# Kernel optimization log

Hardware: AMD Instinct MI355X
Metric: run time of the kernel (lower is better)

Reference implementation:

```python
import jax, jax.numpy as jnp
import numpy as np

P = 9          # patch_size (hardcoded in module)
P2 = P * P     # 81


def _conv1x1(t, W, b):
    # t: (B, C, D, H, W); 1x1x1 Conv3d == per-voxel channel mix
    return jnp.einsum('bcdhw,oc->bodhw', t, W) + b[None, :, None, None, None]


def _unfold_patches(t, nD, nW):
    # t: (C, D, HW) -> non-overlapping P x P patches, torch.nn.Unfold ordering
    C = t.shape[0]
    t = t.reshape(C, nD, P, nW, P)            # (C, pd, kd, pw, kw)
    t = t.transpose(0, 1, 3, 2, 4)            # (C, pd, pw, kd, kw)
    return t.reshape(C, nD * nW, P2)          # (C, L, 81)


def _res_trans(v, W1, W2):
    # Sequential(Linear(81->162, no bias), Linear(162->81, no bias), LeakyReLU(0.2))
    h = jnp.einsum('clk,mk->clm', v, W1)      # (C, L, 162)
    h = jnp.einsum('clm,km->clk', h, W2)      # (C, L, 81)
    return jax.nn.leaky_relu(h, negative_slope=0.2)


def setup_inputs() -> dict:
    key = jax.random.key(0)
    ks = jax.random.split(key, 8)
    B, C, D, H, W = 1, 32, 36, 48, 48
    return {
        'x': jax.random.normal(ks[0], (B, C, D, H, W), jnp.float32),
        'y': jax.random.normal(ks[1], (B, C, D, H, W), jnp.float32),
        'W_img': jax.random.normal(ks[2], (C, C), jnp.float32) * 0.05,
        'b_img': jax.random.normal(ks[3], (C,), jnp.float32) * 0.05,
        'W_fea': jax.random.normal(ks[4], (C, C), jnp.float32) * 0.05,
        'b_fea': jax.random.normal(ks[5], (C,), jnp.float32) * 0.05,
        'W1': jax.random.normal(ks[6], (2 * P2, P2), jnp.float32) * 0.05,
        'W2': jax.random.normal(ks[7], (P2, 2 * P2), jnp.float32) * 0.05,
    }


def reference(x, y, W_img, b_img, W_fea, b_fea, W1, W2):
    B, C, D, H, W = x.shape
    HW = H * W
    nD, nW = D // P, HW // P
    xc = _conv1x1(x, W_img, b_img).reshape(C, D, HW)
    yc = _conv1x1(y, W_fea, b_fea).reshape(C, D, HW)
    px = _res_trans(_unfold_patches(xc, nD, nW), W1, W2)   # (C, L, 81)
    py = _res_trans(_unfold_patches(yc, nD, nW), W1, W2)   # (C, L, 81)
    # att[c, l1, l2] = <px[c,l1], py[c,l2]> / 81  (vectorized over channels)
    att = jnp.einsum('clk,cmk->clm', px, py) / P2           # (C, L, L)
    return att[None]                                        # (1, C, L, L)
```

## Files before the change

kernel.cpp:

```cpp
#include <hip/hip_runtime.h>
#include <hip/hip_bf16.h>

typedef unsigned short u16;
using short8  = __attribute__((ext_vector_type(8))) short;
using floatx4 = __attribute__((ext_vector_type(4))) float;

#define KPAD 104
#define VSTR 96

__device__ __forceinline__ u16 f2bf(float f) {
  union { float f; unsigned u; } v; v.f = f;
  unsigned r = v.u + 0x7fffu + ((v.u >> 16) & 1u);
  return (u16)(r >> 16);
}

__global__ __launch_bounds__(256) void k_conv(const float* __restrict__ xg,
                                              const float* __restrict__ yg,
                                              const float* __restrict__ Wi,
                                              const float* __restrict__ bi,
                                              const float* __restrict__ Wf,
                                              const float* __restrict__ bfe,
                                              const float* __restrict__ W1,
                                              const float* __restrict__ W2,
                                              u16* __restrict__ V,
                                              u16* __restrict__ wepad) {
  int t = threadIdx.x;
  if (blockIdx.y == 2) {
    if (blockIdx.x >= 39) return;
    int idx = blockIdx.x * 256 + t;
    int kp = idx / 104, k = idx - kp * 104;
    float s = 0.f;
    if (kp < 81 && k < 81) {
      #pragma unroll 6
      for (int m = 0; m < 162; ++m)
        s = fmaf(W2[kp * 162 + m], W1[m * 81 + k], s);
    }
    wepad[idx] = (kp < 81 && k < 81) ? f2bf(s) : (u16)0;
    return;
  }
  __shared__ float Ws[1024];
  __shared__ float bs[32];
  int tensor = blockIdx.y;
  const float* src = tensor ? yg : xg;
  const float* Wg  = tensor ? Wf : Wi;
  const float* bg  = tensor ? bfe : bi;
  for (int i = t; i < 1024; i += 256) Ws[i] = Wg[i];
  if (t < 32) bs[t] = bg[t];
  __syncthreads();

  int vbase = blockIdx.x * 512 + t;
  float xin[2][32];
  #pragma unroll
  for (int c = 0; c < 32; ++c) {
    xin[0][c] = src[c * 82944 + vbase];
    xin[1][c] = src[c * 82944 + vbase + 256];
  }
  int dst[2];
  #pragma unroll
  for (int v = 0; v < 2; ++v) {
    int vox = vbase + v * 256;
    int d  = vox / 2304, hw = vox - d * 2304;
    int pd = d / 9,  kd = d  - pd * 9;
    int pw = hw / 9, kw = hw - pw * 9;
    dst[v] = tensor * (32 * 1024 * VSTR) + (pd * 256 + pw) * VSTR + kd * 9 + kw;
  }
  #pragma unroll
  for (int o = 0; o < 32; ++o) {
    float s0 = bs[o], s1 = bs[o];
    #pragma unroll
    for (int c = 0; c < 32; ++c) {
      float w = Ws[o * 32 + c];
      s0 = fmaf(w, xin[0][c], s0);
      s1 = fmaf(w, xin[1][c], s1);
    }
    V[dst[0] + o * (1024 * VSTR)] = f2bf(s0);
    V[dst[1] + o * (1024 * VSTR)] = f2bf(s1);
  }
}

__global__ __launch_bounds__(256, 2) void k_att(const u16* __restrict__ V,
                                                const u16* __restrict__ wepad,
                                                float* __restrict__ out) {
  __shared__ u16 WeT[96 * KPAD];
  __shared__ u16 pxs[128 * KPAD];
  __shared__ u16 pys[128 * KPAD];
  int t = threadIdx.x;
  int c = blockIdx.z;
  int l1b = blockIdx.y * 128, l2b = blockIdx.x * 128;
  const u16* vx = V + ((c)      * 1024 + l1b) * VSTR;
  const u16* vy = V + ((32 + c) * 1024 + l2b) * VSTR;

  for (int i = t; i < 1248; i += 256)
    *(short8*)&WeT[i * 8] = ((const short8*)wepad)[i];
  for (int i = t; i < 1536; i += 256) {
    int r = i / 12, xx = i - r * 12;
    short8 a = *(const short8*)&vx[i * 8];
    short8 b = *(const short8*)&vy[i * 8];
    *(short8*)&pxs[r * KPAD + xx * 8] = a;
    *(short8*)&pys[r * KPAD + xx * 8] = b;
  }
  __syncthreads();

  int wave = t >> 6, lane = t & 63;
  int m15 = lane & 15, quad = lane >> 4;

  short8 bw[6][3];
  #pragma unroll
  for (int j = 0; j < 6; ++j)
    #pragma unroll
    for (int ks = 0; ks < 3; ++ks)
      bw[j][ks] = *(const short8*)&WeT[(j * 16 + m15) * KPAD + ks * 32 + quad * 8];

  int wbase = wave * 32;
  #pragma unroll
  for (int tz = 0; tz < 2; ++tz) {
    u16* buf = tz ? pys : pxs;
    short8 a[2][3];
    #pragma unroll
    for (int i2 = 0; i2 < 2; ++i2)
      #pragma unroll
      for (int ks = 0; ks < 3; ++ks)
        a[i2][ks] = *(const short8*)&buf[(wbase + i2 * 16 + m15) * KPAD + ks * 32 + quad * 8];
    floatx4 pacc[2][6];
    #pragma unroll
    for (int i2 = 0; i2 < 2; ++i2)
      #pragma unroll
      for (int j = 0; j < 6; ++j) pacc[i2][j] = (floatx4){0.f, 0.f, 0.f, 0.f};
    #pragma unroll
    for (int ks = 0; ks < 3; ++ks)
      #pragma unroll
      for (int i2 = 0; i2 < 2; ++i2)
        #pragma unroll
        for (int j = 0; j < 6; ++j)
          pacc[i2][j] = __builtin_amdgcn_mfma_f32_16x16x32_bf16(a[i2][ks], bw[j][ks], pacc[i2][j], 0, 0, 0);
    #pragma unroll
    for (int i2 = 0; i2 < 2; ++i2)
      #pragma unroll
      for (int j = 0; j < 6; ++j)
        #pragma unroll
        for (int reg = 0; reg < 4; ++reg) {
          int row = wbase + i2 * 16 + quad * 4 + reg;
          int col = j * 16 + m15;
          float v = pacc[i2][j][reg];
          v = v > 0.f ? v : 0.2f * v;
          buf[row * KPAD + col] = f2bf(v);
        }
  }
  __syncthreads();

  int wy = (wave >> 1) * 64, wx = (wave & 1) * 64;
  floatx4 acc[4][4];
  #pragma unroll
  for (int i = 0; i < 4; ++i)
    #pragma unroll
    for (int j = 0; j < 4; ++j) acc[i][j] = (floatx4){0.f, 0.f, 0.f, 0.f};

  #pragma unroll
  for (int ks = 0; ks < 3; ++ks) {
    short8 a[4], b[4];
    #pragma unroll
    for (int i = 0; i < 4; ++i)
      a[i] = *(const short8*)&pxs[(wy + i * 16 + m15) * KPAD + ks * 32 + quad * 8];
    #pragma unroll
    for (int j = 0; j < 4; ++j)
      b[j] = *(const short8*)&pys[(wx + j * 16 + m15) * KPAD + ks * 32 + quad * 8];
    #pragma unroll
    for (int i = 0; i < 4; ++i)
      #pragma unroll
      for (int j = 0; j < 4; ++j)
        acc[i][j] = __builtin_amdgcn_mfma_f32_16x16x32_bf16(a[i], b[j], acc[i][j], 0, 0, 0);
  }

  const float inv = 1.f / 81.f;
  #pragma unroll
  for (int i = 0; i < 4; ++i)
    #pragma unroll
    for (int j = 0; j < 4; ++j)
      #pragma unroll
      for (int reg = 0; reg < 4; ++reg) {
        int row = l1b + wy + i * 16 + quad * 4 + reg;
        int col = l2b + wx + j * 16 + m15;
        out[(c << 20) + (row << 10) + col] = acc[i][j][reg] * inv;
      }
}

extern "C" void kernel_launch(void* const* d_in, const int* in_sizes, int n_in,
                              void* d_out, int out_size, void* d_ws, size_t ws_size,
                              hipStream_t stream) {
  const float* x    = (const float*)d_in[0];
  const float* y    = (const float*)d_in[1];
  const float* Wimg = (const float*)d_in[2];
  const float* bimg = (const float*)d_in[3];
  const float* Wfea = (const float*)d_in[4];
  const float* bfea = (const float*)d_in[5];
  const float* W1   = (const float*)d_in[6];
  const float* W2   = (const float*)d_in[7];
  float* out = (float*)d_out;

  char* ws = (char*)d_ws;
  u16* wepad = (u16*)ws;
  u16* V     = (u16*)(ws + 32768);

  hipMemsetAsync(V, 0, 65536 * (size_t)VSTR * 2, stream);
  k_conv<<<dim3(162, 3), 256, 0, stream>>>(x, y, Wimg, bimg, Wfea, bfea, W1, W2, V, wepad);
  k_att<<<dim3(8, 8, 32), 256, 0, stream>>>(V, wepad, out);
}
```

Baseline: 205.4 us.

## Fuse patch projection into conv kernel and drop memset from pipeline

Moves the per-patch Linear+LeakyReLU projection out of the attention kernel and into a new fused conv kernel that computes the 1x1 conv for 4 patches per block directly into shared memory, projects them with MFMA and writes the projected patches to global. The attention kernel then only loads the precomputed patches and does the final GEMM. Previously each projection was recomputed 8 times across attention tiles. The change also removes the workspace memset by zeroing the padding in shared memory, and raises attention occupancy to 3 blocks per CU. It adds a third launch and uses strided, less coalesced input reads in the fused conv.

New measurement: 201.7 us. Within noise of the previous version (-1.8%).

```diff
diff --git a/kernel.cpp b/kernel.cpp
--- a/kernel.cpp
+++ b/kernel.cpp
@@ -1,5 +1,4 @@
 #include <hip/hip_runtime.h>
-#include <hip/hip_bf16.h>
 
 typedef unsigned short u16;
 using short8  = __attribute__((ext_vector_type(8))) short;
@@ -14,84 +13,132 @@
   return (u16)(r >> 16);
 }
 
-__global__ __launch_bounds__(256) void k_conv(const float* __restrict__ xg,
-                                              const float* __restrict__ yg,
-                                              const float* __restrict__ Wi,
-                                              const float* __restrict__ bi,
-                                              const float* __restrict__ Wf,
-                                              const float* __restrict__ bfe,
-                                              const float* __restrict__ W1,
+__global__ __launch_bounds__(256) void k_weff(const float* __restrict__ W1,
                                               const float* __restrict__ W2,
-                                              u16* __restrict__ V,
                                               u16* __restrict__ wepad) {
-  int t = threadIdx.x;
-  if (blockIdx.y == 2) {
-    if (blockIdx.x >= 39) return;
-    int idx = blockIdx.x * 256 + t;
-    int kp = idx / 104, k = idx - kp * 104;
-    float s = 0.f;
-    if (kp < 81 && k < 81) {
-      #pragma unroll 6
-      for (int m = 0; m < 162; ++m)
-        s = fmaf(W2[kp * 162 + m], W1[m * 81 + k], s);
-    }
-    wepad[idx] = (kp < 81 && k < 81) ? f2bf(s) : (u16)0;
-    return;
-  }
+  int idx = blockIdx.x * 256 + threadIdx.x;
+  if (idx >= 96 * 104) return;
+  int kp = idx / 104, k = idx - kp * 104;
+  float s = 0.f;
+  if (kp < 81 && k < 81) {
+    #pragma unroll 6
+    for (int m = 0; m < 162; ++m)
+      s = fmaf(W2[kp * 162 + m], W1[m * 81 + k], s);
+  }
+  wepad[idx] = (kp < 81 && k < 81) ? f2bf(s) : (u16)0;
+}
+
+__global__ __launch_bounds__(256, 2) void k_fused(const float* __restrict__ xg,
+                                                  const float* __restrict__ yg,
+                                                  const float* __restrict__ Wi,
+                                                  const float* __restrict__ bi,
+                                                  const float* __restrict__ Wf,
+                                                  const float* __restrict__ bfe,
+                                                  const u16* __restrict__ wepad,
+                                                  u16* __restrict__ Pg) {
   __shared__ float Ws[1024];
   __shared__ float bs[32];
+  __shared__ u16 WeT[96 * KPAD];
+  __shared__ u16 Vs[128 * KPAD];
+  int t = threadIdx.x;
   int tensor = blockIdx.y;
+  int g = blockIdx.x;
   const float* src = tensor ? yg : xg;
   const float* Wg  = tensor ? Wf : Wi;
   const float* bg  = tensor ? bfe : bi;
+
   for (int i = t; i < 1024; i += 256) Ws[i] = Wg[i];
   if (t < 32) bs[t] = bg[t];
-  __syncthreads();
-
-  int vbase = blockIdx.x * 512 + t;
-  float xin[2][32];
-  #pragma unroll
-  for (int c = 0; c < 32; ++c) {
-    xin[0][c] = src[c * 82944 + vbase];
-    xin[1][c] = src[c * 82944 + vbase + 256];
-  }
-  int dst[2];
-  #pragma unroll
-  for (int v = 0; v < 2; ++v) {
-    int vox = vbase + v * 256;
-    int d  = vox / 2304, hw = vox - d * 2304;
-    int pd = d / 9,  kd = d  - pd * 9;
-    int pw = hw / 9, kw = hw - pw * 9;
-    dst[v] = tensor * (32 * 1024 * VSTR) + (pd * 256 + pw) * VSTR + kd * 9 + kw;
-  }
-  #pragma unroll
-  for (int o = 0; o < 32; ++o) {
-    float s0 = bs[o], s1 = bs[o];
-    #pragma unroll
-    for (int c = 0; c < 32; ++c) {
-      float w = Ws[o * 32 + c];
-      s0 = fmaf(w, xin[0][c], s0);
-      s1 = fmaf(w, xin[1][c], s1);
+  for (int i = t; i < 1248; i += 256)
+    *(short8*)&WeT[i * 8] = ((const short8*)wepad)[i];
+  if (t < 128) {
+    #pragma unroll
+    for (int cc = 81; cc < 96; ++cc) Vs[t * KPAD + cc] = 0;
+  }
+  __syncthreads();
+
+  int l0 = g * 4;
+  int pd = l0 >> 8, pw0 = l0 & 255;
+  #pragma unroll
+  for (int it = 0; it < 2; ++it) {
+    int vox = t + it * 256;
+    if (vox < 324) {
+      int lp = vox / 81, k = vox - lp * 81;
+      int kd = k / 9, kw = k - kd * 9;
+      const float* sp = src + (pd * 9 + kd) * 2304 + (pw0 + lp) * 9 + kw;
+      float xin[32];
+      #pragma unroll
+      for (int c2 = 0; c2 < 32; ++c2) xin[c2] = sp[c2 * 82944];
+      #pragma unroll
+      for (int o = 0; o < 32; ++o) {
+        float s = bs[o];
+        #pragma unroll
+        for (int c2 = 0; c2 < 32; ++c2) s = fmaf(Ws[o * 32 + c2], xin[c2], s);
+        Vs[(o * 4 + lp) * KPAD + k] = f2bf(s);
+      }
     }
-    V[dst[0] + o * (1024 * VSTR)] = f2bf(s0);
-    V[dst[1] + o * (1024 * VSTR)] = f2bf(s1);
-  }
-}
-
-__global__ __launch_bounds__(256, 2) void k_att(const u16* __restrict__ V,
-                                                const u16* __restrict__ wepad,
+  }
+  __syncthreads();
+
+  int wave = t >> 6, lane = t & 63;
+  int m15 = lane & 15, quad = lane >> 4;
+  short8 bw[6][3];
+  #pragma unroll
+  for (int j = 0; j < 6; ++j)
+    #pragma unroll
+    for (int ks = 0; ks < 3; ++ks)
+      bw[j][ks] = *(const short8*)&WeT[(j * 16 + m15) * KPAD + ks * 32 + quad * 8];
+  int wbase = wave * 32;
+  short8 a[2][3];
+  #pragma unroll
+  for (int i2 = 0; i2 < 2; ++i2)
+    #pragma unroll
+    for (int ks = 0; ks < 3; ++ks)
+      a[i2][ks] = *(const short8*)&Vs[(wbase + i2 * 16 + m15) * KPAD + ks * 32 + quad * 8];
+  floatx4 pacc[2][6];
+  #pragma unroll
+  for (int i2 = 0; i2 < 2; ++i2)
+    #pragma unroll
+    for (int j = 0; j < 6; ++j) pacc[i2][j] = (floatx4){0.f, 0.f, 0.f, 0.f};
+  #pragma unroll
+  for (int ks = 0; ks < 3; ++ks)
+    #pragma unroll
+    for (int i2 = 0; i2 < 2; ++i2)
+      #pragma unroll
+      for (int j = 0; j < 6; ++j)
+        pacc[i2][j] = __builtin_amdgcn_mfma_f32_16x16x32_bf16(a[i2][ks], bw[j][ks], pacc[i2][j], 0, 0, 0);
+  #pragma unroll
+  for (int i2 = 0; i2 < 2; ++i2)
+    #pragma unroll
+    for (int j = 0; j < 6; ++j)
+      #pragma unroll
+      for (int reg = 0; reg < 4; ++reg) {
+        int row = wbase + i2 * 16 + quad * 4 + reg;
+        int col = j * 16 + m15;
+        float v = pacc[i2][j][reg];
+        v = v > 0.f ? v : 0.2f * v;
+        Vs[row * KPAD + col] = f2bf(v);
+      }
+  __syncthreads();
+
+  for (int i = t; i < 1536; i += 256) {
+    int r = i / 12, xx = i - r * 12;
+    int o = r >> 2, lp = r & 3;
+    size_t row = (size_t)(tensor * 32 + o) * 1024 + (l0 + lp);
+    *(short8*)&Pg[row * VSTR + xx * 8] = *(const short8*)&Vs[r * KPAD + xx * 8];
+  }
+}
+
+__global__ __launch_bounds__(256, 3) void k_att(const u16* __restrict__ P,
                                                 float* __restrict__ out) {
-  __shared__ u16 WeT[96 * KPAD];
   __shared__ u16 pxs[128 * KPAD];
   __shared__ u16 pys[128 * KPAD];
   int t = threadIdx.x;
   int c = blockIdx.z;
   int l1b = blockIdx.y * 128, l2b = blockIdx.x * 128;
-  const u16* vx = V + ((c)      * 1024 + l1b) * VSTR;
-  const u16* vy = V + ((32 + c) * 1024 + l2b) * VSTR;
-
-  for (int i = t; i < 1248; i += 256)
-    *(short8*)&WeT[i * 8] = ((const short8*)wepad)[i];
+  const u16* vx = P + ((size_t)c        * 1024 + l1b) * VSTR;
+  const u16* vy = P + ((size_t)(32 + c) * 1024 + l2b) * VSTR;
+
   for (int i = t; i < 1536; i += 256) {
     int r = i / 12, xx = i - r * 12;
     short8 a = *(const short8*)&vx[i * 8];
@@ -103,51 +150,6 @@
 
   int wave = t >> 6, lane = t & 63;
   int m15 = lane & 15, quad = lane >> 4;
-
-  short8 bw[6][3];
-  #pragma unroll
-  for (int j = 0; j < 6; ++j)
-    #pragma unroll
-    for (int ks = 0; ks < 3; ++ks)
-      bw[j][ks] = *(const short8*)&WeT[(j * 16 + m15) * KPAD + ks * 32 + quad * 8];
-
-  int wbase = wave * 32;
-  #pragma unroll
-  for (int tz = 0; tz < 2; ++tz) {
-    u16* buf = tz ? pys : pxs;
-    short8 a[2][3];
-    #pragma unroll
-    for (int i2 = 0; i2 < 2; ++i2)
-      #pragma unroll
-      for (int ks = 0; ks < 3; ++ks)
-        a[i2][ks] = *(const short8*)&buf[(wbase + i2 * 16 + m15) * KPAD + ks * 32 + quad * 8];
-    floatx4 pacc[2][6];
-    #pragma unroll
-    for (int i2 = 0; i2 < 2; ++i2)
-      #pragma unroll
-      for (int j = 0; j < 6; ++j) pacc[i2][j] = (floatx4){0.f, 0.f, 0.f, 0.f};
-    #pragma unroll
-    for (int ks = 0; ks < 3; ++ks)
-      #pragma unroll
-      for (int i2 = 0; i2 < 2; ++i2)
-        #pragma unroll
-        for (int j = 0; j < 6; ++j)
-          pacc[i2][j] = __builtin_amdgcn_mfma_f32_16x16x32_bf16(a[i2][ks], bw[j][ks], pacc[i2][j], 0, 0, 0);
-    #pragma unroll
-    for (int i2 = 0; i2 < 2; ++i2)
-      #pragma unroll
-      for (int j = 0; j < 6; ++j)
-        #pragma unroll
-        for (int reg = 0; reg < 4; ++reg) {
-          int row = wbase + i2 * 16 + quad * 4 + reg;
-          int col = j * 16 + m15;
-          float v = pacc[i2][j][reg];
-          v = v > 0.f ? v : 0.2f * v;
-          buf[row * KPAD + col] = f2bf(v);
-        }
-  }
-  __syncthreads();
-
   int wy = (wave >> 1) * 64, wx = (wave & 1) * 64;
   floatx4 acc[4][4];
   #pragma unroll
@@ -199,9 +201,9 @@
 
   char* ws = (char*)d_ws;
   u16* wepad = (u16*)ws;
-  u16* V     = (u16*)(ws + 32768);
-
-  hipMemsetAsync(V, 0, 65536 * (size_t)VSTR * 2, stream);
-  k_conv<<<dim3(162, 3), 256, 0, stream>>>(x, y, Wimg, bimg, Wfea, bfea, W1, W2, V, wepad);
-  k_att<<<dim3(8, 8, 32), 256, 0, stream>>>(V, wepad, out);
-}
+  u16* Pg    = (u16*)(ws + 32768);
+
+  k_weff <<<dim3(39),       256, 0, stream>>>(W1, W2, wepad);
+  k_fused<<<dim3(256, 2),   256, 0, stream>>>(x, y, Wimg, bimg, Wfea, bfea, wepad, Pg);
+  k_att  <<<dim3(8, 8, 32), 256, 0, stream>>>(Pg, out);
+}
```
